# Kernel optimization log

Hardware: AMD Instinct MI355X
Metric: run time of the kernel (lower is better)

Reference implementation:

```python
import jax, jax.numpy as jnp
import numpy as np

B, T, E = 4, 2048, 1024
H, KV = 16, 4          # query heads, key/value heads
D = E // H             # head_dim = 64
G = H // KV            # query heads per kv head = 4
NEG = -1e9


def setup_inputs() -> dict:
    key = jax.random.key(0)
    ks = jax.random.split(key, 6)
    hidden_states = jax.random.normal(ks[0], (B, T, E), dtype=jnp.float32)
    # additive causal mask [B, 1, T, T]
    causal = jnp.where(jnp.tril(jnp.ones((T, T), dtype=bool)), 0.0, NEG).astype(jnp.float32)
    attention_mask = jnp.broadcast_to(causal[None, None], (B, 1, T, T))
    s = 0.02
    Wq = jax.random.normal(ks[1], (E, E), dtype=jnp.float32) * s
    Wk = jax.random.normal(ks[2], (E, KV * D), dtype=jnp.float32) * s
    Wv = jax.random.normal(ks[3], (E, KV * D), dtype=jnp.float32) * s
    Wo = jax.random.normal(ks[4], (E, E), dtype=jnp.float32) * s
    bq = jnp.zeros((E,), jnp.float32)
    bk = jnp.zeros((KV * D,), jnp.float32)
    bv = jnp.zeros((KV * D,), jnp.float32)
    bo = jnp.zeros((E,), jnp.float32)
    return {"hidden_states": hidden_states, "attention_mask": attention_mask,
            "Wq": Wq, "bq": bq, "Wk": Wk, "bk": bk, "Wv": Wv, "bv": bv,
            "Wo": Wo, "bo": bo}


def reference(hidden_states, attention_mask, Wq, bq, Wk, bk, Wv, bv, Wo, bo):
    b, t, e = hidden_states.shape
    scaling = D ** -0.5
    # projections (torch Linear: x @ W + b with W stored [in, out])
    q = (hidden_states @ Wq + bq) * scaling           # [b, t, E]
    k = hidden_states @ Wk + bk                        # [b, t, KV*D]
    v = hidden_states @ Wv + bv
    # [b, KV, G, t, D] for q; [b, KV, t, D] for k/v (GQA grouping == repeat_kv math)
    q = q.reshape(b, t, KV, G, D).transpose(0, 2, 3, 1, 4)
    k = k.reshape(b, t, KV, D).transpose(0, 2, 1, 3)
    v = v.reshape(b, t, KV, D).transpose(0, 2, 1, 3)
    scores = jnp.einsum('bkgsd,bktd->bkgst', q, k)     # [b, KV, G, t, t]
    scores = scores + attention_mask[:, :, None, :, :]  # broadcast [b,1,1,t,t]
    w = jax.nn.softmax(scores, axis=-1)
    out = jnp.einsum('bkgst,bktd->bkgsd', w, v)        # [b, KV, G, t, D]
    out = out.transpose(0, 3, 1, 2, 4).reshape(b, t, e)  # heads back to embed
    return out @ Wo + bo
```

## Files before the change

kernel.cpp:

```cpp
#include <hip/hip_runtime.h>

typedef __bf16 bf16;
typedef __attribute__((ext_vector_type(8))) __bf16 bf16x8;
typedef __attribute__((ext_vector_type(4))) __bf16 bf16x4;
typedef __attribute__((ext_vector_type(4))) float f32x4;

#define B_ 4
#define T_ 2048
#define E_ 1024
#define H_ 16
#define KV_ 4
#define D_ 64
#define KVD_ 256
#define QKVS_ 1536
#define M_ 8192

#define MASK_NEG (-3.0e4f)
#define QSCALE (0.125f * 1.4426950408889634f)

__device__ inline bf16x8 load8(const bf16* p) { return *(const bf16x8*)p; }
__device__ inline bf16x8 load8(const float* p) {
  f32x4 a = *(const f32x4*)p;
  f32x4 b = *(const f32x4*)(p + 4);
  bf16x8 r;
#pragma unroll
  for (int j = 0; j < 4; ++j) { r[j] = (bf16)a[j]; r[4 + j] = (bf16)b[j]; }
  return r;
}

__device__ inline void gload_lds16(const bf16* g, bf16* l) {
  __builtin_amdgcn_global_load_lds(
      (const __attribute__((address_space(1))) void*)g,
      (__attribute__((address_space(3))) void*)l, 16, 0, 0);
}

__global__ __launch_bounds__(256) void cast_k(const float* __restrict__ src,
                                              bf16* __restrict__ dst) {
  size_t i = ((size_t)blockIdx.x * 256 + threadIdx.x) * 8;
  *(bf16x8*)(dst + i) = load8(src + i);
}

__global__ __launch_bounds__(256) void wprep_k(const float* __restrict__ Wq,
                                               const float* __restrict__ Wk,
                                               const float* __restrict__ Wv,
                                               const float* __restrict__ Wo,
                                               bf16* __restrict__ WqkvT,
                                               bf16* __restrict__ WoT) {
  const int z = blockIdx.z;
  const float* W;
  bf16* WT;
  int N;
  if (z == 0) { W = Wq; WT = WqkvT; N = 1024; }
  else if (z == 1) { W = Wo; WT = WoT; N = 1024; }
  else if (z == 2) { if (blockIdx.y >= 8) return; W = Wk; WT = WqkvT + 1024 * 1024; N = 256; }
  else { if (blockIdx.y >= 8) return; W = Wv; WT = WqkvT + 1280 * 1024; N = 256; }

  __shared__ bf16 tile[32][33];
  int k0 = blockIdx.x * 32, n0 = blockIdx.y * 32;
  int tr = threadIdx.x >> 5;
  int tc = threadIdx.x & 31;
#pragma unroll
  for (int i = 0; i < 32; i += 8)
    tile[tr + i][tc] = (bf16)W[(size_t)(k0 + tr + i) * N + n0 + tc];
  __syncthreads();
#pragma unroll
  for (int i = 0; i < 32; i += 8)
    WT[(size_t)(n0 + tr + i) * 1024 + k0 + tc] = tile[tc][tr + i];
}

__global__ __launch_bounds__(256) void vtrans_k(const bf16* __restrict__ src,
                                                bf16* __restrict__ dst) {
  __shared__ bf16 tile[32][33];
  int r0 = blockIdx.x * 32;
  int c0 = blockIdx.y * 32;
  int tr = threadIdx.x >> 5, tc = threadIdx.x & 31;
#pragma unroll
  for (int i = 0; i < 32; i += 8)
    tile[tr + i][tc] = src[(size_t)(r0 + tr + i) * QKVS_ + 1280 + c0 + tc];
  __syncthreads();
#pragma unroll
  for (int i = 0; i < 32; i += 8) {
    int c = c0 + tr + i;
    int r = r0 + tc;
    dst[(size_t)((r >> 11) * KVD_ + c) * T_ + (r & (T_ - 1))] = tile[tc][tr + i];
  }
}

__global__ __launch_bounds__(256) void qkv_gemm_k(const bf16* __restrict__ A,
                                                  const bf16* __restrict__ WT,
                                                  const float* __restrict__ bq,
                                                  const float* __restrict__ bk,
                                                  const float* __restrict__ bv,
                                                  bf16* __restrict__ C) {
  const int K = E_;
  const int m0 = blockIdx.x * 128;
  const int n0 = blockIdx.y * 128;
  const int tid = threadIdx.x;
  const int wave = tid >> 6;
  const int lane = tid & 63;
  const int wr = wave >> 1;
  const int wc = wave & 1;
  const int fr = lane & 15;
  const int quad = lane >> 4;

  __shared__ bf16 sA[128][32];
  __shared__ bf16 sB[128][32];

  f32x4 acc[4][4] = {};

  const int ldr = lane >> 2;
  const int ldk = (lane & 3) * 8;
  const bf16* Ag0 = A + (size_t)(m0 + wave * 32 + ldr) * K + ldk;
  const bf16* Ag1 = Ag0 + (size_t)16 * K;
  const bf16* Bg0 = WT + (size_t)(n0 + wave * 32 + ldr) * K + ldk;
  const bf16* Bg1 = Bg0 + (size_t)16 * K;
  bf16* sA0 = &sA[wave * 32][0];
  bf16* sA1 = &sA[wave * 32 + 16][0];
  bf16* sB0 = &sB[wave * 32][0];
  bf16* sB1 = &sB[wave * 32 + 16][0];

  for (int k0 = 0; k0 < K; k0 += 32) {
    gload_lds16(Ag0 + k0, sA0);
    gload_lds16(Ag1 + k0, sA1);
    gload_lds16(Bg0 + k0, sB0);
    gload_lds16(Bg1 + k0, sB1);
    __syncthreads();

    bf16x8 af[4], bfr[4];
#pragma unroll
    for (int m = 0; m < 4; ++m)
      af[m] = *(const bf16x8*)(&sA[wr * 64 + m * 16 + fr][quad * 8]);
#pragma unroll
    for (int n = 0; n < 4; ++n)
      bfr[n] = *(const bf16x8*)(&sB[wc * 64 + n * 16 + fr][quad * 8]);
#pragma unroll
    for (int m = 0; m < 4; ++m)
#pragma unroll
      for (int n = 0; n < 4; ++n)
        acc[m][n] = __builtin_amdgcn_mfma_f32_16x16x32_bf16(af[m], bfr[n], acc[m][n], 0, 0, 0);
    __syncthreads();
  }

#pragma unroll
  for (int n = 0; n < 4; ++n) {
    int col = n0 + wc * 64 + n * 16 + fr;
    float bias, sc;
    if (col < 1024) { bias = bq[col]; sc = QSCALE; }
    else if (col < 1280) { bias = bk[col - 1024]; sc = 1.f; }
    else { bias = bv[col - 1280]; sc = 1.f; }
#pragma unroll
    for (int m = 0; m < 4; ++m) {
#pragma unroll
      for (int i = 0; i < 4; ++i) {
        int row = m0 + wr * 64 + m * 16 + quad * 4 + i;
        C[(size_t)row * QKVS_ + col] = (bf16)((acc[m][n][i] + bias) * sc);
      }
    }
  }
}

__global__ __launch_bounds__(256) void gemm128_k(const bf16* __restrict__ A,
                                                 const bf16* __restrict__ WT,
                                                 const float* __restrict__ bias,
                                                 float* __restrict__ C,
                                                 int M, int N, int K) {
  const int m0 = blockIdx.x * 128;
  const int n0 = blockIdx.y * 128;
  const int tid = threadIdx.x;
  const int wave = tid >> 6;
  const int lane = tid & 63;
  const int wr = wave >> 1;
  const int wc = wave & 1;
  const int fr = lane & 15;
  const int quad = lane >> 4;

  __shared__ bf16 sA[128][32];
  __shared__ bf16 sB[128][32];

  f32x4 acc[4][4] = {};

  const int ldr = lane >> 2;
  const int ldk = (lane & 3) * 8;
  const bf16* Ag0 = A + (size_t)(m0 + wave * 32 + ldr) * K + ldk;
  const bf16* Ag1 = Ag0 + (size_t)16 * K;
  const bf16* Bg0 = WT + (size_t)(n0 + wave * 32 + ldr) * K + ldk;
  const bf16* Bg1 = Bg0 + (size_t)16 * K;
  bf16* sA0 = &sA[wave * 32][0];
  bf16* sA1 = &sA[wave * 32 + 16][0];
  bf16* sB0 = &sB[wave * 32][0];
  bf16* sB1 = &sB[wave * 32 + 16][0];

  for (int k0 = 0; k0 < K; k0 += 32) {
    gload_lds16(Ag0 + k0, sA0);
    gload_lds16(Ag1 + k0, sA1);
    gload_lds16(Bg0 + k0, sB0);
    gload_lds16(Bg1 + k0, sB1);
    __syncthreads();

    bf16x8 af[4], bfr[4];
#pragma unroll
    for (int m = 0; m < 4; ++m)
      af[m] = *(const bf16x8*)(&sA[wr * 64 + m * 16 + fr][quad * 8]);
#pragma unroll
    for (int n = 0; n < 4; ++n)
      bfr[n] = *(const bf16x8*)(&sB[wc * 64 + n * 16 + fr][quad * 8]);
#pragma unroll
    for (int m = 0; m < 4; ++m)
#pragma unroll
      for (int n = 0; n < 4; ++n)
        acc[m][n] = __builtin_amdgcn_mfma_f32_16x16x32_bf16(af[m], bfr[n], acc[m][n], 0, 0, 0);
    __syncthreads();
  }

#pragma unroll
  for (int n = 0; n < 4; ++n) {
    int col = n0 + wc * 64 + n * 16 + fr;
    float bv = bias[col];
#pragma unroll
    for (int m = 0; m < 4; ++m) {
#pragma unroll
      for (int i = 0; i < 4; ++i) {
        int row = m0 + wr * 64 + m * 16 + quad * 4 + i;
        C[(size_t)row * N + col] = (acc[m][n][i] + bv);
      }
    }
  }
}

__global__ __launch_bounds__(256) void attn_k(const bf16* __restrict__ QKVg,
                                              const bf16* __restrict__ VTg,
                                              bf16* __restrict__ Og) {
  const int jp = blockIdx.x;
  const int h = blockIdx.y;
  const int b = blockIdx.z;
  const int kv = h >> 2;
  const int tid = threadIdx.x;
  const int wave = tid >> 6;
  const int lane = tid & 63;
  const int fr = lane & 15;
  const int quad = lane >> 4;

  __shared__ bf16 Ks[64][72];
  __shared__ bf16 Vt[64][72];
  __shared__ bf16 Pt[64][72];

  const int skey = tid & 63;
  const int sdc = (tid >> 6) * 16;
  const int svd = tid >> 2;
  const int svk = (tid & 3) * 16;
  const bf16* kbase = QKVg + (size_t)(b * T_ + skey) * QKVS_ + 1024 + kv * 64 + sdc;
  const bf16* vbase = VTg + (size_t)((b * KV_ + kv) * D_ + svd) * T_ + svk;

  for (int ph = 0; ph < 2; ++ph) {
    const int qb = ph ? (31 - jp) : jp;

    bf16x8 qa0, qa1;
    {
      const bf16* qsrc = QKVg + (size_t)(b * T_ + qb * 64 + wave * 16 + fr) * QKVS_ + h * 64 + quad * 8;
      qa0 = *(const bf16x8*)(qsrc);
      qa1 = *(const bf16x8*)(qsrc + 32);
    }

    f32x4 Oacc[4] = {};
    float m_run = MASK_NEG, l_run = 0.f;

    bf16x8 k0p, k1p, v0p, v1p;
    k0p = *(const bf16x8*)(kbase);
    k1p = *(const bf16x8*)(kbase + 8);
    v0p = *(const bf16x8*)(vbase);
    v1p = *(const bf16x8*)(vbase + 8);

    for (int kb = 0; kb <= qb; ++kb) {
      *(bf16x8*)(&Ks[skey][sdc]) = k0p;
      *(bf16x8*)(&Ks[skey][sdc + 8]) = k1p;
      *(bf16x8*)(&Vt[svd][svk]) = v0p;
      *(bf16x8*)(&Vt[svd][svk + 8]) = v1p;
      __syncthreads();

      if (kb < qb) {
        const bf16* kp = kbase + (size_t)(kb + 1) * 64 * QKVS_;
        const bf16* vp = vbase + (size_t)(kb + 1) * 64;
        k0p = *(const bf16x8*)(kp);
        k1p = *(const bf16x8*)(kp + 8);
        v0p = *(const bf16x8*)(vp);
        v1p = *(const bf16x8*)(vp + 8);
      } else if (ph == 0) {
        k0p = *(const bf16x8*)(kbase);
        k1p = *(const bf16x8*)(kbase + 8);
        v0p = *(const bf16x8*)(vbase);
        v1p = *(const bf16x8*)(vbase + 8);
      }

      f32x4 S[4] = {};
      __builtin_amdgcn_s_setprio(1);
#pragma unroll
      for (int nt = 0; nt < 4; ++nt) {
        bf16x8 kf0 = *(const bf16x8*)(&Ks[nt * 16 + fr][quad * 8]);
        bf16x8 kf1 = *(const bf16x8*)(&Ks[nt * 16 + fr][32 + quad * 8]);
        S[nt] = __builtin_amdgcn_mfma_f32_16x16x32_bf16(kf0, qa0, S[nt], 0, 0, 0);
        S[nt] = __builtin_amdgcn_mfma_f32_16x16x32_bf16(kf1, qa1, S[nt], 0, 0, 0);
      }
      __builtin_amdgcn_s_setprio(0);

      if (kb == qb) {
        const int ql = wave * 16 + fr;
#pragma unroll
        for (int nt = 0; nt < 4; ++nt)
#pragma unroll
          for (int i = 0; i < 4; ++i)
            if (nt * 16 + quad * 4 + i > ql) S[nt][i] = MASK_NEG;
      }

      float pm = S[0][0];
#pragma unroll
      for (int nt = 0; nt < 4; ++nt)
#pragma unroll
        for (int i = 0; i < 4; ++i) pm = fmaxf(pm, S[nt][i]);
      pm = fmaxf(pm, __shfl_xor(pm, 16, 64));
      pm = fmaxf(pm, __shfl_xor(pm, 32, 64));
      if (pm > m_run) {
        float al = exp2f(m_run - pm);
        m_run = pm;
        l_run *= al;
#pragma unroll
        for (int dt = 0; dt < 4; ++dt)
#pragma unroll
          for (int i = 0; i < 4; ++i) Oacc[dt][i] *= al;
      }
      float ps = 0.f;
#pragma unroll
      for (int nt = 0; nt < 4; ++nt)
#pragma unroll
        for (int i = 0; i < 4; ++i) {
          float p = exp2f(S[nt][i] - m_run);
          S[nt][i] = p;
          ps += p;
        }
      ps += __shfl_xor(ps, 16, 64);
      ps += __shfl_xor(ps, 32, 64);
      l_run += ps;

#pragma unroll
      for (int nt = 0; nt < 4; ++nt) {
        bf16x4 w;
#pragma unroll
        for (int i = 0; i < 4; ++i) w[i] = (bf16)S[nt][i];
        *(bf16x4*)(&Pt[wave * 16 + fr][nt * 16 + quad * 4]) = w;
      }
      __threadfence_block();

      bf16x8 pb0 = *(const bf16x8*)(&Pt[wave * 16 + fr][quad * 8]);
      bf16x8 pb1 = *(const bf16x8*)(&Pt[wave * 16 + fr][32 + quad * 8]);
      __builtin_amdgcn_s_setprio(1);
#pragma unroll
      for (int dt = 0; dt < 4; ++dt) {
        bf16x8 vf0 = *(const bf16x8*)(&Vt[dt * 16 + fr][quad * 8]);
        bf16x8 vf1 = *(const bf16x8*)(&Vt[dt * 16 + fr][32 + quad * 8]);
        Oacc[dt] = __builtin_amdgcn_mfma_f32_16x16x32_bf16(vf0, pb0, Oacc[dt], 0, 0, 0);
        Oacc[dt] = __builtin_amdgcn_mfma_f32_16x16x32_bf16(vf1, pb1, Oacc[dt], 0, 0, 0);
      }
      __builtin_amdgcn_s_setprio(0);
      __syncthreads();
    }

    {
      float inv = 1.f / fmaxf(l_run, 1e-30f);
      bf16* dst = Og + (size_t)(b * T_ + qb * 64 + wave * 16 + fr) * E_ + h * 64;
#pragma unroll
      for (int dt = 0; dt < 4; ++dt) {
        bf16x4 o;
#pragma unroll
        for (int i = 0; i < 4; ++i) o[i] = (bf16)(Oacc[dt][i] * inv);
        *(bf16x4*)(dst + dt * 16 + quad * 4) = o;
      }
    }
  }
}

extern "C" void kernel_launch(void* const* d_in, const int* in_sizes, int n_in,
                              void* d_out, int out_size, void* d_ws, size_t ws_size,
                              hipStream_t stream) {
  (void)in_sizes; (void)n_in; (void)out_size; (void)ws_size;
  const float* hidden = (const float*)d_in[0];
  const float* Wq = (const float*)d_in[2];
  const float* bq = (const float*)d_in[3];
  const float* Wk = (const float*)d_in[4];
  const float* bk = (const float*)d_in[5];
  const float* Wv = (const float*)d_in[6];
  const float* bv = (const float*)d_in[7];
  const float* Wo = (const float*)d_in[8];
  const float* bo = (const float*)d_in[9];
  float* out = (float*)d_out;

  char* ws = (char*)d_ws;
  bf16* WqkvT = (bf16*)(ws);
  bf16* WoT   = (bf16*)(ws + (3u << 20));
  bf16* QKVb  = (bf16*)(ws + (5u << 20));
  bf16* Hb    = (bf16*)(ws + (29u << 20));
  bf16* Ab    = (bf16*)(ws + (29u << 20));
  bf16* VbT   = (bf16*)(ws + (45u << 20));

  cast_k<<<dim3(M_ * E_ / (256 * 8)), 256, 0, stream>>>(hidden, Hb);
  wprep_k<<<dim3(32, 32, 4), 256, 0, stream>>>(Wq, Wk, Wv, Wo, WqkvT, WoT);

  qkv_gemm_k<<<dim3(64, 12), 256, 0, stream>>>(Hb, WqkvT, bq, bk, bv, QKVb);

  vtrans_k<<<dim3(256, 8), 256, 0, stream>>>(QKVb, VbT);

  attn_k<<<dim3(16, 16, 4), 256, 0, stream>>>(QKVb, VbT, Ab);

  gemm128_k<<<dim3(64, 8), 256, 0, stream>>>(Ab, WoT, bo, out, M_, E_, E_);
}
```

Baseline: 285.6 us.

## Fuse fp32-to-bf16 hidden cast into QKV GEMM and widen K tile

Removes the separate cast kernel and has the QKV GEMM read fp32 hidden states directly, converting to bf16 in registers with a one-iteration register prefetch before storing to LDS. Both GEMMs move from a K-step of 32 to 64, halving the number of barrier pairs, and gain a launch_bounds occupancy hint of 3 blocks. This saves a full 8192x1024 bf16 write and reread plus one launch. In exchange the A operand now travels as fp32, doubling its global traffic inside the GEMM. The unpadded 64-wide LDS rows may also cause bank conflicts on the fragment reads.

```diff
diff --git a/kernel.cpp b/kernel.cpp
--- a/kernel.cpp
+++ b/kernel.cpp
@@ -19,25 +19,11 @@
 #define QSCALE (0.125f * 1.4426950408889634f)
 
 __device__ inline bf16x8 load8(const bf16* p) { return *(const bf16x8*)p; }
-__device__ inline bf16x8 load8(const float* p) {
-  f32x4 a = *(const f32x4*)p;
-  f32x4 b = *(const f32x4*)(p + 4);
-  bf16x8 r;
-#pragma unroll
-  for (int j = 0; j < 4; ++j) { r[j] = (bf16)a[j]; r[4 + j] = (bf16)b[j]; }
-  return r;
-}
 
 __device__ inline void gload_lds16(const bf16* g, bf16* l) {
   __builtin_amdgcn_global_load_lds(
       (const __attribute__((address_space(1))) void*)g,
       (__attribute__((address_space(3))) void*)l, 16, 0, 0);
-}
-
-__global__ __launch_bounds__(256) void cast_k(const float* __restrict__ src,
-                                              bf16* __restrict__ dst) {
-  size_t i = ((size_t)blockIdx.x * 256 + threadIdx.x) * 8;
-  *(bf16x8*)(dst + i) = load8(src + i);
 }
 
 __global__ __launch_bounds__(256) void wprep_k(const float* __restrict__ Wq,
@@ -86,12 +72,12 @@
   }
 }
 
-__global__ __launch_bounds__(256) void qkv_gemm_k(const bf16* __restrict__ A,
-                                                  const bf16* __restrict__ WT,
-                                                  const float* __restrict__ bq,
-                                                  const float* __restrict__ bk,
-                                                  const float* __restrict__ bv,
-                                                  bf16* __restrict__ C) {
+__global__ __launch_bounds__(256, 3) void qkv_gemm_k(const float* __restrict__ A,
+                                                     const bf16* __restrict__ WT,
+                                                     const float* __restrict__ bq,
+                                                     const float* __restrict__ bk,
+                                                     const float* __restrict__ bv,
+                                                     bf16* __restrict__ C) {
   const int K = E_;
   const int m0 = blockIdx.x * 128;
   const int n0 = blockIdx.y * 128;
@@ -103,41 +89,67 @@
   const int fr = lane & 15;
   const int quad = lane >> 4;
 
-  __shared__ bf16 sA[128][32];
-  __shared__ bf16 sB[128][32];
+  __shared__ bf16 sA[128 * 64];
+  __shared__ bf16 sB[128 * 64];
 
   f32x4 acc[4][4] = {};
 
-  const int ldr = lane >> 2;
-  const int ldk = (lane & 3) * 8;
-  const bf16* Ag0 = A + (size_t)(m0 + wave * 32 + ldr) * K + ldk;
-  const bf16* Ag1 = Ag0 + (size_t)16 * K;
-  const bf16* Bg0 = WT + (size_t)(n0 + wave * 32 + ldr) * K + ldk;
-  const bf16* Bg1 = Bg0 + (size_t)16 * K;
-  bf16* sA0 = &sA[wave * 32][0];
-  bf16* sA1 = &sA[wave * 32 + 16][0];
-  bf16* sB0 = &sB[wave * 32][0];
-  bf16* sB1 = &sB[wave * 32 + 16][0];
-
-  for (int k0 = 0; k0 < K; k0 += 32) {
-    gload_lds16(Ag0 + k0, sA0);
-    gload_lds16(Ag1 + k0, sA1);
-    gload_lds16(Bg0 + k0, sB0);
-    gload_lds16(Bg1 + k0, sB1);
+  const int ar = tid >> 3;
+  const int ac = (tid & 7) * 8;
+  const float* Agp = A + (size_t)(m0 + ar) * K + ac;
+  bf16* sAw = sA + tid * 8;
+
+  const int br = lane >> 3;
+  const int bc = (lane & 7) * 8;
+  const bf16* Bgp = WT + (size_t)(n0 + wave * 32 + br) * K + bc;
+  bf16* sBw = sB + (size_t)(wave * 4) * 512;
+
+  f32x4 a_pre[8];
+#pragma unroll
+  for (int s = 0; s < 4; ++s) {
+    a_pre[2 * s] = *(const f32x4*)(Agp + (size_t)32 * s * K);
+    a_pre[2 * s + 1] = *(const f32x4*)(Agp + (size_t)32 * s * K + 4);
+  }
+
+  for (int k0 = 0; k0 < K; k0 += 64) {
+#pragma unroll
+    for (int s = 0; s < 4; ++s) {
+      bf16x8 w;
+#pragma unroll
+      for (int j = 0; j < 4; ++j) {
+        w[j] = (bf16)a_pre[2 * s][j];
+        w[4 + j] = (bf16)a_pre[2 * s + 1][j];
+      }
+      *(bf16x8*)(sAw + s * 2048) = w;
+    }
+#pragma unroll
+    for (int j = 0; j < 4; ++j)
+      gload_lds16(Bgp + (size_t)8 * j * K + k0, sBw + j * 512);
     __syncthreads();
 
-    bf16x8 af[4], bfr[4];
-#pragma unroll
-    for (int m = 0; m < 4; ++m)
-      af[m] = *(const bf16x8*)(&sA[wr * 64 + m * 16 + fr][quad * 8]);
-#pragma unroll
-    for (int n = 0; n < 4; ++n)
-      bfr[n] = *(const bf16x8*)(&sB[wc * 64 + n * 16 + fr][quad * 8]);
-#pragma unroll
-    for (int m = 0; m < 4; ++m)
+    if (k0 + 64 < K) {
+#pragma unroll
+      for (int s = 0; s < 4; ++s) {
+        a_pre[2 * s] = *(const f32x4*)(Agp + (size_t)32 * s * K + k0 + 64);
+        a_pre[2 * s + 1] = *(const f32x4*)(Agp + (size_t)32 * s * K + k0 + 68);
+      }
+    }
+
+#pragma unroll
+    for (int kk = 0; kk < 2; ++kk) {
+      bf16x8 af[4], bfr[4];
+#pragma unroll
+      for (int m = 0; m < 4; ++m)
+        af[m] = *(const bf16x8*)(sA + (size_t)(wr * 64 + m * 16 + fr) * 64 + kk * 32 + quad * 8);
 #pragma unroll
       for (int n = 0; n < 4; ++n)
-        acc[m][n] = __builtin_amdgcn_mfma_f32_16x16x32_bf16(af[m], bfr[n], acc[m][n], 0, 0, 0);
+        bfr[n] = *(const bf16x8*)(sB + (size_t)(wc * 64 + n * 16 + fr) * 64 + kk * 32 + quad * 8);
+#pragma unroll
+      for (int m = 0; m < 4; ++m)
+#pragma unroll
+        for (int n = 0; n < 4; ++n)
+          acc[m][n] = __builtin_amdgcn_mfma_f32_16x16x32_bf16(af[m], bfr[n], acc[m][n], 0, 0, 0);
+    }
     __syncthreads();
   }
 
@@ -159,11 +171,11 @@
   }
 }
 
-__global__ __launch_bounds__(256) void gemm128_k(const bf16* __restrict__ A,
-                                                 const bf16* __restrict__ WT,
-                                                 const float* __restrict__ bias,
-                                                 float* __restrict__ C,
-                                                 int M, int N, int K) {
+__global__ __launch_bounds__(256, 3) void gemm128_k(const bf16* __restrict__ A,
+                                                    const bf16* __restrict__ WT,
+                                                    const float* __restrict__ bias,
+                                                    float* __restrict__ C,
+                                                    int M, int N, int K) {
   const int m0 = blockIdx.x * 128;
   const int n0 = blockIdx.y * 128;
   const int tid = threadIdx.x;
@@ -174,41 +186,41 @@
   const int fr = lane & 15;
   const int quad = lane >> 4;
 
-  __shared__ bf16 sA[128][32];
-  __shared__ bf16 sB[128][32];
+  __shared__ bf16 sA[128 * 64];
+  __shared__ bf16 sB[128 * 64];
 
   f32x4 acc[4][4] = {};
 
-  const int ldr = lane >> 2;
-  const int ldk = (lane & 3) * 8;
-  const bf16* Ag0 = A + (size_t)(m0 + wave * 32 + ldr) * K + ldk;
-  const bf16* Ag1 = Ag0 + (size_t)16 * K;
-  const bf16* Bg0 = WT + (size_t)(n0 + wave * 32 + ldr) * K + ldk;
-  const bf16* Bg1 = Bg0 + (size_t)16 * K;
-  bf16* sA0 = &sA[wave * 32][0];
-  bf16* sA1 = &sA[wave * 32 + 16][0];
-  bf16* sB0 = &sB[wave * 32][0];
-  bf16* sB1 = &sB[wave * 32 + 16][0];
-
-  for (int k0 = 0; k0 < K; k0 += 32) {
-    gload_lds16(Ag0 + k0, sA0);
-    gload_lds16(Ag1 + k0, sA1);
-    gload_lds16(Bg0 + k0, sB0);
-    gload_lds16(Bg1 + k0, sB1);
+  const int lr = lane >> 3;
+  const int lc = (lane & 7) * 8;
+  const bf16* Agp = A + (size_t)(m0 + wave * 32 + lr) * K + lc;
+  const bf16* Bgp = WT + (size_t)(n0 + wave * 32 + lr) * K + lc;
+  bf16* sAw = sA + (size_t)(wave * 4) * 512;
+  bf16* sBw = sB + (size_t)(wave * 4) * 512;
+
+  for (int k0 = 0; k0 < K; k0 += 64) {
+#pragma unroll
+    for (int j = 0; j < 4; ++j) {
+      gload_lds16(Agp + (size_t)8 * j * K + k0, sAw + j * 512);
+      gload_lds16(Bgp + (size_t)8 * j * K + k0, sBw + j * 512);
+    }
     __syncthreads();
 
-    bf16x8 af[4], bfr[4];
-#pragma unroll
-    for (int m = 0; m < 4; ++m)
-      af[m] = *(const bf16x8*)(&sA[wr * 64 + m * 16 + fr][quad * 8]);
-#pragma unroll
-    for (int n = 0; n < 4; ++n)
-      bfr[n] = *(const bf16x8*)(&sB[wc * 64 + n * 16 + fr][quad * 8]);
-#pragma unroll
-    for (int m = 0; m < 4; ++m)
+#pragma unroll
+    for (int kk = 0; kk < 2; ++kk) {
+      bf16x8 af[4], bfr[4];
+#pragma unroll
+      for (int m = 0; m < 4; ++m)
+        af[m] = *(const bf16x8*)(sA + (size_t)(wr * 64 + m * 16 + fr) * 64 + kk * 32 + quad * 8);
 #pragma unroll
       for (int n = 0; n < 4; ++n)
-        acc[m][n] = __builtin_amdgcn_mfma_f32_16x16x32_bf16(af[m], bfr[n], acc[m][n], 0, 0, 0);
+        bfr[n] = *(const bf16x8*)(sB + (size_t)(wc * 64 + n * 16 + fr) * 64 + kk * 32 + quad * 8);
+#pragma unroll
+      for (int m = 0; m < 4; ++m)
+#pragma unroll
+        for (int n = 0; n < 4; ++n)
+          acc[m][n] = __builtin_amdgcn_mfma_f32_16x16x32_bf16(af[m], bfr[n], acc[m][n], 0, 0, 0);
+    }
     __syncthreads();
   }
 
@@ -396,14 +408,12 @@
   bf16* WqkvT = (bf16*)(ws);
   bf16* WoT   = (bf16*)(ws + (3u << 20));
   bf16* QKVb  = (bf16*)(ws + (5u << 20));
-  bf16* Hb    = (bf16*)(ws + (29u << 20));
   bf16* Ab    = (bf16*)(ws + (29u << 20));
   bf16* VbT   = (bf16*)(ws + (45u << 20));
 
-  cast_k<<<dim3(M_ * E_ / (256 * 8)), 256, 0, stream>>>(hidden, Hb);
   wprep_k<<<dim3(32, 32, 4), 256, 0, stream>>>(Wq, Wk, Wv, Wo, WqkvT, WoT);
 
-  qkv_gemm_k<<<dim3(64, 12), 256, 0, stream>>>(Hb, WqkvT, bq, bk, bv, QKVb);
+  qkv_gemm_k<<<dim3(64, 12), 256, 0, stream>>>(hidden, WqkvT, bq, bk, bv, QKVb);
 
   vtrans_k<<<dim3(256, 8), 256, 0, stream>>>(QKVb, VbT);
 
```

Result: no change. 287.2 us (+0.6%).

## Merge cast and weight prep kernels; remap block IDs for XCD-aware locality

Applied to the files above, without the earlier changes.

Folds the hidden-state cast into the weight transpose/prep kernel by adding extra z-slices, removing one kernel launch. Remaps linear block IDs in the QKV GEMM, output GEMM and attention kernels so that consecutive original tiles land on the same XCD (round-robin by 8). The aim is better L2 reuse of shared A/B panels and K/V data within each XCD. The remapping assumes the grid sizes are multiples of 8 and that the hardware dispatches blocks round-robin across 8 XCDs.

```diff
diff --git a/kernel.cpp b/kernel.cpp
--- a/kernel.cpp
+++ b/kernel.cpp
@@ -34,19 +34,21 @@
       (__attribute__((address_space(3))) void*)l, 16, 0, 0);
 }
 
-__global__ __launch_bounds__(256) void cast_k(const float* __restrict__ src,
-                                              bf16* __restrict__ dst) {
-  size_t i = ((size_t)blockIdx.x * 256 + threadIdx.x) * 8;
-  *(bf16x8*)(dst + i) = load8(src + i);
-}
-
-__global__ __launch_bounds__(256) void wprep_k(const float* __restrict__ Wq,
-                                               const float* __restrict__ Wk,
-                                               const float* __restrict__ Wv,
-                                               const float* __restrict__ Wo,
-                                               bf16* __restrict__ WqkvT,
-                                               bf16* __restrict__ WoT) {
+__global__ __launch_bounds__(256) void prep_k(const float* __restrict__ hidden,
+                                              bf16* __restrict__ Hb,
+                                              const float* __restrict__ Wq,
+                                              const float* __restrict__ Wk,
+                                              const float* __restrict__ Wv,
+                                              const float* __restrict__ Wo,
+                                              bf16* __restrict__ WqkvT,
+                                              bf16* __restrict__ WoT) {
   const int z = blockIdx.z;
+  if (z >= 4) {
+    size_t lin = (size_t)blockIdx.x + 32 * blockIdx.y + 1024 * (z - 4);
+    size_t i = lin * 2048 + (size_t)threadIdx.x * 8;
+    *(bf16x8*)(Hb + i) = load8(hidden + i);
+    return;
+  }
   const float* W;
   bf16* WT;
   int N;
@@ -93,8 +95,10 @@
                                                   const float* __restrict__ bv,
                                                   bf16* __restrict__ C) {
   const int K = E_;
-  const int m0 = blockIdx.x * 128;
-  const int n0 = blockIdx.y * 128;
+  const int dsp = blockIdx.x + 64 * blockIdx.y;
+  const int orig = (dsp & 7) * 96 + (dsp >> 3);
+  const int m0 = (orig & 63) * 128;
+  const int n0 = (orig >> 6) * 128;
   const int tid = threadIdx.x;
   const int wave = tid >> 6;
   const int lane = tid & 63;
@@ -164,8 +168,10 @@
                                                  const float* __restrict__ bias,
                                                  float* __restrict__ C,
                                                  int M, int N, int K) {
-  const int m0 = blockIdx.x * 128;
-  const int n0 = blockIdx.y * 128;
+  const int dsp = blockIdx.x + 64 * blockIdx.y;
+  const int orig = (dsp & 7) * 64 + (dsp >> 3);
+  const int m0 = (orig & 63) * 128;
+  const int n0 = (orig >> 6) * 128;
   const int tid = threadIdx.x;
   const int wave = tid >> 6;
   const int lane = tid & 63;
@@ -230,9 +236,11 @@
 __global__ __launch_bounds__(256) void attn_k(const bf16* __restrict__ QKVg,
                                               const bf16* __restrict__ VTg,
                                               bf16* __restrict__ Og) {
-  const int jp = blockIdx.x;
-  const int h = blockIdx.y;
-  const int b = blockIdx.z;
+  const int dsp = blockIdx.x + 16 * blockIdx.y + 256 * blockIdx.z;
+  const int orig = (dsp & 7) * 128 + (dsp >> 3);
+  const int jp = orig & 15;
+  const int h = (orig >> 4) & 15;
+  const int b = orig >> 8;
   const int kv = h >> 2;
   const int tid = threadIdx.x;
   const int wave = tid >> 6;
@@ -400,8 +408,7 @@
   bf16* Ab    = (bf16*)(ws + (29u << 20));
   bf16* VbT   = (bf16*)(ws + (45u << 20));
 
-  cast_k<<<dim3(M_ * E_ / (256 * 8)), 256, 0, stream>>>(hidden, Hb);
-  wprep_k<<<dim3(32, 32, 4), 256, 0, stream>>>(Wq, Wk, Wv, Wo, WqkvT, WoT);
+  prep_k<<<dim3(32, 32, 8), 256, 0, stream>>>(hidden, Hb, Wq, Wk, Wv, Wo, WqkvT, WoT);
 
   qkv_gemm_k<<<dim3(64, 12), 256, 0, stream>>>(Hb, WqkvT, bq, bk, bv, QKVb);
 
```

Result: slower. 301.9 us (+5.7%).
